# Kernel tuning notes

Measured on AMD Instinct MI355X. Metric: run time of the kernel, lower is better.

The kernel has to match this reference:

```python
import jax, jax.numpy as jnp
import numpy as np

B, S, D, H, V = 4, 1024, 1024, 16, 1024
HD = D // H  # head_dim = 64
FF = 4 * D


def _layer_norm(x, g, b, eps=1e-5):
    mu = jnp.mean(x, axis=-1, keepdims=True)
    var = jnp.var(x, axis=-1, keepdims=True)
    return (x - mu) * jax.lax.rsqrt(var + eps) * g + b


def _pos_encoding(seq_len, d_model):
    # sinusoidal PE, matching PositionalEncoding buffer construction
    pos = jnp.arange(seq_len, dtype=jnp.float32)[:, None]
    div = jnp.exp(jnp.arange(0, d_model, 2, dtype=jnp.float32) * (-np.log(10000.0) / d_model))
    pe = jnp.zeros((seq_len, d_model), dtype=jnp.float32)
    pe = pe.at[:, 0::2].set(jnp.sin(pos * div))
    pe = pe.at[:, 1::2].set(jnp.cos(pos * div))
    return pe


def setup_inputs() -> dict:
    key = jax.random.key(0)
    ks = jax.random.split(key, 12)
    sc = 0.02
    return {
        "inputs": jax.random.randint(ks[0], (B, S), 0, V, dtype=jnp.int32),
        "targets": jax.random.randint(ks[1], (B, S), 0, V, dtype=jnp.int32),
        "wte": jax.random.normal(ks[2], (V, D), jnp.float32) * sc,
        "wq": jax.random.normal(ks[3], (D, D), jnp.float32) * sc,
        "bq": jnp.zeros((D,), jnp.float32),
        "wk": jax.random.normal(ks[4], (D, D), jnp.float32) * sc,
        "bk": jnp.zeros((D,), jnp.float32),
        "wv": jax.random.normal(ks[5], (D, D), jnp.float32) * sc,
        "bv": jnp.zeros((D,), jnp.float32),
        "wo": jax.random.normal(ks[6], (D, D), jnp.float32) * sc,
        "bo": jnp.zeros((D,), jnp.float32),
        "w1": jax.random.normal(ks[7], (D, FF), jnp.float32) * sc,
        "b1": jnp.zeros((FF,), jnp.float32),
        "w2": jax.random.normal(ks[8], (FF, D), jnp.float32) * sc,
        "b2": jnp.zeros((D,), jnp.float32),
        "ln1_g": jnp.ones((D,), jnp.float32),
        "ln1_b": jnp.zeros((D,), jnp.float32),
        "ln2_g": jnp.ones((D,), jnp.float32),
        "ln2_b": jnp.zeros((D,), jnp.float32),
    }


def reference(inputs, targets, wte, wq, bq, wk, bk, wv, bv, wo, bo,
              w1, b1, w2, b2, ln1_g, ln1_b, ln2_g, ln2_b):
    # embedding + positional encoding
    x = wte[inputs] + _pos_encoding(S, D)  # [B,S,D]

    # naive causal multi-head attention (dropout = identity in eval)
    q = (x @ wq + bq).reshape(B, S, H, HD)
    k = (x @ wk + bk).reshape(B, S, H, HD)
    v = (x @ wv + bv).reshape(B, S, H, HD)
    scores = jnp.einsum('bqhd,bkhd->bhqk', q, k) / np.sqrt(HD)  # [B,H,S,S]
    causal = jnp.tril(jnp.ones((S, S), dtype=bool))
    scores = jnp.where(causal, scores, -jnp.inf)
    attn = jax.nn.softmax(scores, axis=-1)
    ctx = jnp.einsum('bhqk,bkhd->bqhd', attn, v).reshape(B, S, D)
    att_out = ctx @ wo + bo

    # residual + LN1, FFN + GELU, residual + LN2
    adn = _layer_norm(x + att_out, ln1_g, ln1_b)
    h = jax.nn.gelu(adn @ w1 + b1, approximate=False) @ w2 + b2
    logits = _layer_norm(h + adn, ln2_g, ln2_b)

    # cross-entropy over d_model(=vocab) classes
    logits_flat = logits.reshape(B * S, D)
    tgt = targets.reshape(B * S)
    logp = jax.nn.log_softmax(logits_flat, axis=-1)
    loss = -jnp.mean(jnp.take_along_axis(logp, tgt[:, None], axis=-1))
    return logits_flat, loss
```

## Files before the change

kernel.cpp:

```cpp
#include <hip/hip_runtime.h>
#include <math.h>

#define BB 4
#define SS 1024
#define DD 1024
#define HH 16
#define HDIM 64
#define FF 4096
#define MM 4096

typedef short bf16x8 __attribute__((ext_vector_type(8)));
typedef short bf16x4 __attribute__((ext_vector_type(4)));
typedef float f32x4  __attribute__((ext_vector_type(4)));

static __device__ __forceinline__ short f2bf(float f){
  unsigned u = __float_as_uint(f);
  u += 0x7FFFu + ((u >> 16) & 1u);
  return (short)(u >> 16);
}
static __device__ __forceinline__ float b2f(short s){
  return __uint_as_float(((unsigned)(unsigned short)s) << 16);
}

static __device__ __forceinline__ float erf_fast(float x){
  float ax = fabsf(x);
  float t  = __builtin_amdgcn_rcpf(1.0f + 0.3275911f * ax);
  float p  = t * (0.254829592f + t * (-0.284496736f + t * (1.421413741f +
             t * (-1.453152027f + t * 1.061405429f))));
  float e  = 1.0f - p * __expf(-ax * ax);
  return copysignf(e, x);
}

static __device__ __forceinline__ void gl_lds16(const short* g, short* l){
  __builtin_amdgcn_global_load_lds((const __attribute__((address_space(1))) unsigned int*)g,
                                   (__attribute__((address_space(3))) unsigned int*)l,
                                   16, 0, 0);
}

__global__ __launch_bounds__(256) void trans_all_kernel(
    const float* __restrict__ wq, const float* __restrict__ wk,
    const float* __restrict__ wv, const float* __restrict__ wo,
    const float* __restrict__ w1, const float* __restrict__ w2,
    short* __restrict__ wqkvt, short* __restrict__ wot,
    short* __restrict__ w1t,   short* __restrict__ w2t){
  __shared__ float t[32][33];
  int idx = blockIdx.x;
  const float* src; short* dst; int R, C, cx, ry;
  if (idx < 4096){
    int wsel = idx >> 10, tt = idx & 1023;
    cx = tt & 31; ry = tt >> 5; R = 1024; C = 1024;
    src = (wsel == 0) ? wq : (wsel == 1) ? wk : (wsel == 2) ? wv : wo;
    dst = (wsel == 3) ? wot : wqkvt + (size_t)wsel * 1024 * 1024;
  } else if (idx < 8192){
    int tt = idx - 4096; cx = tt & 127; ry = tt >> 7; R = 1024; C = 4096;
    src = w1; dst = w1t;
  } else {
    int tt = idx - 8192; cx = tt & 31; ry = tt >> 5; R = 4096; C = 1024;
    src = w2; dst = w2t;
  }
  int c0 = cx * 32, r0 = ry * 32;
  int tx = threadIdx.x, ty = threadIdx.y;
#pragma unroll
  for (int i = 0; i < 32; i += 8)
    t[ty + i][tx] = src[(size_t)(r0 + ty + i) * C + (c0 + tx)];
  __syncthreads();
#pragma unroll
  for (int i = 0; i < 32; i += 8)
    dst[(size_t)(c0 + ty + i) * R + (r0 + tx)] = f2bf(t[tx][ty + i]);
}

__global__ __launch_bounds__(256) void concat_bias_kernel(const float* __restrict__ a,
                                                          const float* __restrict__ b,
                                                          const float* __restrict__ c,
                                                          float* __restrict__ dst){
  int t = blockIdx.x * 256 + threadIdx.x;
  float v = (t < 1024) ? a[t] : (t < 2048 ? b[t - 1024] : c[t - 2048]);
  dst[t] = v;
}

__global__ __launch_bounds__(256) void embed_kernel(const int* __restrict__ inputs,
                                                    const float* __restrict__ wte,
                                                    short* __restrict__ xb){
  int idx4 = blockIdx.x * 256 + threadIdx.x;
  int row = idx4 >> 8;
  int d   = (idx4 & 255) * 4;
  int s   = row & (SS - 1);
  int tok = inputs[row];
  float4 w = *(const float4*)&wte[(size_t)tok * DD + d];
  const float cdiv = -9.210340371976184f / 512.0f;
  int i0 = d >> 1;
  float ang0 = (float)s * expf((float)i0 * cdiv);
  float ang1 = (float)s * expf((float)(i0 + 1) * cdiv);
  float x0 = w.x + sinf(ang0);
  float x1 = w.y + cosf(ang0);
  float x2 = w.z + sinf(ang1);
  float x3 = w.w + cosf(ang1);
  bf16x4 sb; sb[0]=f2bf(x0); sb[1]=f2bf(x1); sb[2]=f2bf(x2); sb[3]=f2bf(x3);
  *(bf16x4*)&xb[(size_t)row * DD + d] = sb;
}

template<int MODE, bool GELU, bool ADDBIAS>
__global__ __launch_bounds__(512) void gemm256_kernel(const short* __restrict__ A,
    const short* __restrict__ Bt, const float* __restrict__ bias,
    short* __restrict__ o0, short* __restrict__ o1,
    short* __restrict__ o2, short* __restrict__ o3,
    short* __restrict__ qo, short* __restrict__ ko, short* __restrict__ vto,
    int M, int N, int K, int Kc){
  __shared__ __align__(16) short lds[4][2][8192];
  int tid = threadIdx.x;
  int lid = blockIdx.y * gridDim.x + blockIdx.x;
  int cpx = (gridDim.x * gridDim.y) >> 3;
  int swz = (lid & 7) * cpx + (lid >> 3);
  int n0 = (swz % gridDim.x) * 256;
  int m0 = (swz / gridDim.x) * 256;
  int bz = blockIdx.z;
  int kbeg = bz * Kc;
  int w = tid >> 6, lane = tid & 63, lr = lane & 15, lg = lane >> 4;
  int wm = w >> 2, wn = w & 3;
  f32x4 acc[8][4] = {};

  int srow = w * 16 + (lane >> 2);
  int scol = (((lane & 3) ^ ((lane >> 3) & 3)) * 8);
  const short* Arow = A  + (size_t)(m0 + srow) * K + kbeg + scol;
  const short* Brow = Bt + (size_t)(n0 + srow) * K + kbeg + scol;

  auto STAGE = [&](int buf, int kt){
    int k0 = kt * 32;
#pragma unroll
    for (int j = 0; j < 2; j++){
      gl_lds16(Arow + (size_t)(j * 128) * K + k0, &lds[buf][0][j * 4096 + w * 512]);
      gl_lds16(Brow + (size_t)(j * 128) * K + k0, &lds[buf][1][j * 4096 + w * 512]);
    }
  };

  int nst = Kc >> 5;
  STAGE(0, 0);
  if (nst > 1) STAGE(1, 1);
  if (nst > 2) STAGE(2, 2);

  int axor = ((lr >> 1) & 3) << 4;

  for (int it = 0; it < nst; it++){
    if (it + 3 < nst) STAGE((it + 3) & 3, it + 3);
    if (it + 3 < nst)      asm volatile("s_waitcnt vmcnt(12)" ::: "memory");
    else if (it + 2 < nst) asm volatile("s_waitcnt vmcnt(8)"  ::: "memory");
    else if (it + 1 < nst) asm volatile("s_waitcnt vmcnt(4)"  ::: "memory");
    else                   asm volatile("s_waitcnt vmcnt(0)"  ::: "memory");
    __builtin_amdgcn_s_barrier();

    const short* la = &lds[it & 3][0][0];
    const short* lb = &lds[it & 3][1][0];
    bf16x8 bfrag[4], afrag[8];
#pragma unroll
    for (int ni = 0; ni < 4; ni++){
      int off = ((((wn * 64 + ni * 16 + lr) * 64) + lg * 16) ^ axor) >> 1;
      bfrag[ni] = *(const bf16x8*)&lb[off];
    }
#pragma unroll
    for (int mi = 0; mi < 8; mi++){
      int off = ((((wm * 128 + mi * 16 + lr) * 64) + lg * 16) ^ axor) >> 1;
      afrag[mi] = *(const bf16x8*)&la[off];
    }
    __builtin_amdgcn_s_setprio(1);
#pragma unroll
    for (int mi = 0; mi < 8; mi++)
#pragma unroll
      for (int ni = 0; ni < 4; ni++)
        acc[mi][ni] = __builtin_amdgcn_mfma_f32_16x16x32_bf16(afrag[mi], bfrag[ni], acc[mi][ni], 0, 0, 0);
    __builtin_amdgcn_s_setprio(0);
    asm volatile("" ::: "memory");
    __builtin_amdgcn_s_barrier();
  }

  short* slab = (MODE == 1) ? ((bz == 0) ? o0 : (bz == 1) ? o1 : (bz == 2) ? o2 : o3) : o0;
  bool addb = ADDBIAS && (MODE != 1 || bz == 0);
#pragma unroll
  for (int mi = 0; mi < 8; mi++){
#pragma unroll
    for (int ni = 0; ni < 4; ni++){
      int ng = n0 + wn * 64 + ni * 16 + lr;
      float bv = addb ? bias[ng] : 0.0f;
      int mg0 = m0 + wm * 128 + mi * 16 + 4 * lg;
      if (MODE == 2){
        int sel = n0 >> 10;
        if (sel == 2){
          int d = ng & 1023; int hh = d >> 6, nn = d & 63;
          int bI = mg0 >> 10, sI = mg0 & 1023;
          bf16x4 pk;
#pragma unroll
          for (int r = 0; r < 4; r++) pk[r] = f2bf(acc[mi][ni][r] + bv);
          *(bf16x4*)&vto[(((size_t)(bI * HH + hh)) * HDIM + nn) * SS + sI] = pk;
        } else {
          short* dst = (sel == 0) ? qo : ko;
#pragma unroll
          for (int r = 0; r < 4; r++)
            dst[(size_t)(mg0 + r) * DD + (ng & 1023)] = f2bf(acc[mi][ni][r] + bv);
        }
      } else {
#pragma unroll
        for (int r = 0; r < 4; r++){
          float v = acc[mi][ni][r] + bv;
          if (GELU) v = 0.5f * v * (1.0f + erf_fast(v * 0.70710678118654752f));
          slab[(size_t)(mg0 + r) * N + ng] = f2bf(v);
        }
      }
    }
  }
}

__global__ __launch_bounds__(256) void attn_kernel(const short* __restrict__ qb,
                                                   const short* __restrict__ kb,
                                                   const short* __restrict__ vtb,
                                                   short* __restrict__ ctxb){
  __shared__ __align__(16) short k_lds[2][64 * 64];
  __shared__ __align__(16) short v_lds[2][64 * 64];
  __shared__ __align__(16) short p_lds[4][2][16 * 72];
  int qp = blockIdx.x, h = blockIdx.y, b = blockIdx.z;
  int Tlo = qp, Thi = 15 - qp;
  int tid = threadIdx.x, w = tid >> 6, lane = tid & 63, lr = lane & 15, lg = lane >> 4;

  const short* kp0 = kb  + (size_t)b * SS * DD + h * HDIM;
  const short* vt0 = vtb + (size_t)(b * HH + h) * HDIM * SS;

  bf16x8 qf0[2], qf1[2];
#pragma unroll
  for (int ti = 0; ti < 2; ti++){
    int T = ti ? Thi : Tlo;
    const short* qp_ = qb + ((size_t)(b * SS + T * 64 + w * 16 + lr) * DD + h * HDIM);
    qf0[ti] = *(const bf16x8*)&qp_[lg * 8];
    qf1[ti] = *(const bf16x8*)&qp_[32 + lg * 8];
  }

  float m[2][4], l[2][4];
  f32x4 acc[2][4] = {};
#pragma unroll
  for (int ti = 0; ti < 2; ti++)
#pragma unroll
    for (int r = 0; r < 4; r++){ m[ti][r] = -1e30f; l[ti][r] = 0.0f; }

  int srow8 = lane >> 3;
  int sjs   = (lane & 7) ^ srow8;
  auto STAGE = [&](int buf, int kt){
#pragma unroll
    for (int i = 0; i < 2; i++){
      int rb  = (w + 4 * i) * 8;
      int row = rb + srow8;
      gl_lds16(kp0 + (size_t)(kt * 64 + row) * DD + sjs * 8, &k_lds[buf][rb * 64]);
      gl_lds16(vt0 + (size_t)row * SS + kt * 64 + sjs * 8,   &v_lds[buf][rb * 64]);
    }
  };

  int cur = 0;
  STAGE(0, 0);
  asm volatile("s_waitcnt vmcnt(0)" ::: "memory");
  __syncthreads();

  bf16x8 pf0[2], pf1[2];
  for (int kt = 0; kt <= Thi; kt++){
    if (kt < Thi) STAGE(cur ^ 1, kt + 1);

    bf16x8 kf0[4], kf1[4];
#pragma unroll
    for (int sub = 0; sub < 4; sub++){
      int r = sub * 16 + lr;
      kf0[sub] = *(const bf16x8*)&k_lds[cur][r * 64 + ((lg     ^ (r & 7)) * 8)];
      kf1[sub] = *(const bf16x8*)&k_lds[cur][r * 64 + (((lg+4) ^ (r & 7)) * 8)];
    }

#pragma unroll
    for (int ti = 0; ti < 2; ti++){
      int T = ti ? Thi : Tlo;
      if (kt > T) continue;
      f32x4 sc4[4];
#pragma unroll
      for (int sub = 0; sub < 4; sub++){
        f32x4 t = {};
        t = __builtin_amdgcn_mfma_f32_16x16x32_bf16(qf0[ti], kf0[sub], t, 0, 0, 0);
        t = __builtin_amdgcn_mfma_f32_16x16x32_bf16(qf1[ti], kf1[sub], t, 0, 0, 0);
#pragma unroll
        for (int r = 0; r < 4; r++) t[r] *= 0.125f;
        sc4[sub] = t;
      }
      if (kt == T){
#pragma unroll
        for (int sub = 0; sub < 4; sub++)
#pragma unroll
          for (int r = 0; r < 4; r++)
            if (16 * sub + lr > 16 * w + 4 * lg + r) sc4[sub][r] = -1e30f;
      }

      float pm[4];
#pragma unroll
      for (int r = 0; r < 4; r++)
        pm[r] = fmaxf(fmaxf(sc4[0][r], sc4[1][r]), fmaxf(sc4[2][r], sc4[3][r]));
#pragma unroll
      for (int off = 1; off < 16; off <<= 1)
#pragma unroll
        for (int r = 0; r < 4; r++) pm[r] = fmaxf(pm[r], __shfl_xor(pm[r], off));

      float scl[4], rs[4];
#pragma unroll
      for (int r = 0; r < 4; r++){
        float mn = fmaxf(m[ti][r], pm[r]);
        scl[r] = __expf(m[ti][r] - mn);
        m[ti][r] = mn;
        rs[r] = 0.0f;
      }
#pragma unroll
      for (int sub = 0; sub < 4; sub++)
#pragma unroll
        for (int r = 0; r < 4; r++){
          float p = __expf(sc4[sub][r] - m[ti][r]);
          sc4[sub][r] = p;
          rs[r] += p;
        }
#pragma unroll
      for (int off = 1; off < 16; off <<= 1)
#pragma unroll
        for (int r = 0; r < 4; r++) rs[r] += __shfl_xor(rs[r], off);
#pragma unroll
      for (int r = 0; r < 4; r++) l[ti][r] = l[ti][r] * scl[r] + rs[r];
#pragma unroll
      for (int nb = 0; nb < 4; nb++)
#pragma unroll
        for (int r = 0; r < 4; r++) acc[ti][nb][r] *= scl[r];

      short* pw = &p_lds[w][ti][0];
#pragma unroll
      for (int sub = 0; sub < 4; sub++)
#pragma unroll
        for (int r = 0; r < 4; r++)
          pw[(4 * lg + r) * 72 + sub * 16 + lr] = f2bf(sc4[sub][r]);
      pf0[ti] = *(const bf16x8*)&pw[lr * 72 + lg * 8];
      pf1[ti] = *(const bf16x8*)&pw[lr * 72 + 32 + lg * 8];
    }

    bf16x8 vf0[4], vf1[4];
#pragma unroll
    for (int nb = 0; nb < 4; nb++){
      int r = nb * 16 + lr;
      vf0[nb] = *(const bf16x8*)&v_lds[cur][r * 64 + ((lg     ^ (r & 7)) * 8)];
      vf1[nb] = *(const bf16x8*)&v_lds[cur][r * 64 + (((lg+4) ^ (r & 7)) * 8)];
    }

#pragma unroll
    for (int ti = 0; ti < 2; ti++){
      int T = ti ? Thi : Tlo;
      if (kt > T) continue;
#pragma unroll
      for (int nb = 0; nb < 4; nb++){
        acc[ti][nb] = __builtin_amdgcn_mfma_f32_16x16x32_bf16(pf0[ti], vf0[nb], acc[ti][nb], 0, 0, 0);
        acc[ti][nb] = __builtin_amdgcn_mfma_f32_16x16x32_bf16(pf1[ti], vf1[nb], acc[ti][nb], 0, 0, 0);
      }
    }

    asm volatile("s_waitcnt vmcnt(0)" ::: "memory");
    __syncthreads();
    cur ^= 1;
  }

#pragma unroll
  for (int ti = 0; ti < 2; ti++){
    int T = ti ? Thi : Tlo;
#pragma unroll
    for (int r = 0; r < 4; r++){
      float inv = 1.0f / l[ti][r];
      int row = T * 64 + w * 16 + 4 * lg + r;
#pragma unroll
      for (int nb = 0; nb < 4; nb++)
        ctxb[(size_t)(b * SS + row) * DD + h * HDIM + nb * 16 + lr] = f2bf(acc[ti][nb][r] * inv);
    }
  }
}

template<int NPART, bool WF32, bool LOSS>
__global__ __launch_bounds__(256) void ln_kernel(const short* __restrict__ p0,
                                                 const short* __restrict__ p1,
                                                 const short* __restrict__ p2,
                                                 const short* __restrict__ p3,
                                                 const short* __restrict__ resb,
                                                 const float* __restrict__ g,
                                                 const float* __restrict__ be,
                                                 float* __restrict__ of,
                                                 short* __restrict__ ob,
                                                 const int* __restrict__ tgt,
                                                 float* __restrict__ lrow){
  int row = blockIdx.x, tid = threadIdx.x;
  size_t base = (size_t)row * DD + tid * 4;
  bf16x4 rv = *(const bf16x4*)&resb[base];
  float x0 = b2f(rv[0]), x1 = b2f(rv[1]), x2 = b2f(rv[2]), x3 = b2f(rv[3]);
  const short* ps[4] = {p0, p1, p2, p3};
#pragma unroll
  for (int p = 0; p < NPART; p++){
    bf16x4 pv = *(const bf16x4*)&ps[p][base];
    x0 += b2f(pv[0]); x1 += b2f(pv[1]); x2 += b2f(pv[2]); x3 += b2f(pv[3]);
  }
  float s = x0 + x1 + x2 + x3;
  float q = x0 * x0 + x1 * x1 + x2 * x2 + x3 * x3;
#pragma unroll
  for (int off = 32; off; off >>= 1){ s += __shfl_xor(s, off); q += __shfl_xor(q, off); }
  __shared__ float red[9];
  if ((tid & 63) == 0){ red[tid >> 6] = s; red[4 + (tid >> 6)] = q; }
  __syncthreads();
  s = red[0] + red[1] + red[2] + red[3];
  q = red[4] + red[5] + red[6] + red[7];
  float mean = s * (1.0f / DD);
  float var  = q * (1.0f / DD) - mean * mean;
  float rstd = rsqrtf(var + 1e-5f);
  float4 gv  = *(const float4*)&g[tid * 4];
  float4 bev = *(const float4*)&be[tid * 4];
  float y0 = (x0 - mean) * rstd * gv.x + bev.x;
  float y1 = (x1 - mean) * rstd * gv.y + bev.y;
  float y2 = (x2 - mean) * rstd * gv.z + bev.z;
  float y3 = (x3 - mean) * rstd * gv.w + bev.w;
  if (WF32){
    *(float4*)&of[base] = make_float4(y0, y1, y2, y3);
  } else {
    bf16x4 sb; sb[0]=f2bf(y0); sb[1]=f2bf(y1); sb[2]=f2bf(y2); sb[3]=f2bf(y3);
    *(bf16x4*)&ob[base] = sb;
  }
  if (LOSS){
    __syncthreads();
    float mx = fmaxf(fmaxf(y0, y1), fmaxf(y2, y3));
#pragma unroll
    for (int off = 32; off; off >>= 1) mx = fmaxf(mx, __shfl_xor(mx, off));
    if ((tid & 63) == 0) red[tid >> 6] = mx;
    int t = tgt[row];
    if (tid == (t >> 2))
      red[8] = ((t & 3) == 0) ? y0 : ((t & 3) == 1) ? y1 : ((t & 3) == 2) ? y2 : y3;
    __syncthreads();
    mx = fmaxf(fmaxf(red[0], red[1]), fmaxf(red[2], red[3]));
    float se = __expf(y0 - mx) + __expf(y1 - mx) + __expf(y2 - mx) + __expf(y3 - mx);
#pragma unroll
    for (int off = 32; off; off >>= 1) se += __shfl_xor(se, off);
    if ((tid & 63) == 0) red[4 + (tid >> 6)] = se;
    __syncthreads();
    if (tid == 0){
      float tot = red[4] + red[5] + red[6] + red[7];
      lrow[row] = mx + logf(tot) - red[8];
    }
  }
}

__global__ __launch_bounds__(256) void loss_reduce_kernel(const float* __restrict__ pr,
                                                          float* __restrict__ outp){
  int tid = threadIdx.x;
  float s = 0.0f;
  for (int i = tid; i < MM; i += 256) s += pr[i];
#pragma unroll
  for (int off = 32; off; off >>= 1) s += __shfl_xor(s, off);
  __shared__ float red[4];
  if ((tid & 63) == 0) red[tid >> 6] = s;
  __syncthreads();
  if (tid == 0) outp[0] = (red[0] + red[1] + red[2] + red[3]) * (1.0f / MM);
}

extern "C" void kernel_launch(void* const* d_in, const int* in_sizes, int n_in,
                              void* d_out, int out_size, void* d_ws, size_t ws_size,
                              hipStream_t stream){
  const int*   inputs  = (const int*)  d_in[0];
  const int*   targets = (const int*)  d_in[1];
  const float* wte     = (const float*)d_in[2];
  const float* wq      = (const float*)d_in[3];
  const float* bq      = (const float*)d_in[4];
  const float* wk      = (const float*)d_in[5];
  const float* bk      = (const float*)d_in[6];
  const float* wv      = (const float*)d_in[7];
  const float* bvv     = (const float*)d_in[8];
  const float* wo      = (const float*)d_in[9];
  const float* bo      = (const float*)d_in[10];
  const float* w1      = (const float*)d_in[11];
  const float* b1      = (const float*)d_in[12];
  const float* w2      = (const float*)d_in[13];
  const float* b2      = (const float*)d_in[14];
  const float* ln1g    = (const float*)d_in[15];
  const float* ln1b    = (const float*)d_in[16];
  const float* ln2g    = (const float*)d_in[17];
  const float* ln2b    = (const float*)d_in[18];
  float* out = (float*)d_out;

  char* ws = (char*)d_ws;
  const size_t MB = 1024 * 1024;
  short* wqkvt = (short*)(ws + 0 * MB);
  short* wot   = (short*)(ws + 6 * MB);
  short* w1t   = (short*)(ws + 8 * MB);
  short* w2t   = (short*)(ws + 16 * MB);
  short* xb    = (short*)(ws + 24 * MB);
  short* qbuf  = (short*)(ws + 32 * MB);
  short* kbuf  = (short*)(ws + 40 * MB);
  short* vtb   = (short*)(ws + 48 * MB);
  short* ctxb  = (short*)(ws + 56 * MB);
  short* pr0   = (short*)(ws + 64 * MB);
  short* pr1   = (short*)(ws + 72 * MB);
  short* pr2   = (short*)(ws + 80 * MB);
  short* pr3   = (short*)(ws + 88 * MB);
  short* adnb  = (short*)(ws + 96 * MB);
  short* h1b   = (short*)(ws + 32 * MB);
  short* hs0   = (short*)(ws + 64 * MB);
  short* hs1   = (short*)(ws + 72 * MB);
  short* hs2   = (short*)(ws + 80 * MB);
  short* hs3   = (short*)(ws + 88 * MB);
  float* lrow  = (float*)(ws + 104 * MB);
  float* bqkv  = (float*)(ws + 105 * MB);

  trans_all_kernel<<<12288, dim3(32, 8), 0, stream>>>(
      wq, wk, wv, wo, w1, w2, wqkvt, wot, w1t, w2t);
  concat_bias_kernel<<<12, 256, 0, stream>>>(bq, bk, bvv, bqkv);

  embed_kernel<<<4096, 256, 0, stream>>>(inputs, wte, xb);

  gemm256_kernel<2, false, true><<<dim3(12, 16), 512, 0, stream>>>(
      xb, wqkvt, bqkv, nullptr, nullptr, nullptr, nullptr,
      qbuf, kbuf, vtb, MM, 3 * DD, DD, DD);

  attn_kernel<<<dim3(8, 16, 4), 256, 0, stream>>>(qbuf, kbuf, vtb, ctxb);

  gemm256_kernel<1, false, true><<<dim3(4, 16, 4), 512, 0, stream>>>(
      ctxb, wot, bo, pr0, pr1, pr2, pr3,
      nullptr, nullptr, nullptr, MM, DD, DD, 256);

  ln_kernel<4, false, false><<<4096, 256, 0, stream>>>(
      pr0, pr1, pr2, pr3, xb, ln1g, ln1b, nullptr, adnb, nullptr, nullptr);

  gemm256_kernel<0, true, true><<<dim3(16, 16), 512, 0, stream>>>(
      adnb, w1t, b1, h1b, nullptr, nullptr, nullptr,
      nullptr, nullptr, nullptr, MM, FF, DD, DD);

  gemm256_kernel<1, false, true><<<dim3(4, 16, 4), 512, 0, stream>>>(
      h1b, w2t, b2, hs0, hs1, hs2, hs3,
      nullptr, nullptr, nullptr, MM, DD, FF, 1024);

  ln_kernel<4, true, true><<<4096, 256, 0, stream>>>(
      hs0, hs1, hs2, hs3, adnb, ln2g, ln2b, out, nullptr, targets, lrow);

  loss_reduce_kernel<<<1, 256, 0, stream>>>(lrow, out + (size_t)MM * DD);
}
```

Before: 237.1 us.

## Double-buffer GEMM fragments in registers and use one barrier per k-step

The GEMM main loop now loads the next k-step's A/B fragments from LDS into a second register set while the MFMAs for the current step run. Each iteration now has one barrier instead of two, and the LDS fragment offsets are computed once before the loop. The launch bounds also ask for two blocks per CU, which caps registers per thread. That cap could force spills, since the accumulators and two fragment sets are held at once, and 128 KB of LDS per block may prevent two blocks from fitting on a CU anyway. The loop also assumes at least three k-stages and an even stage count.

After: 229.4 us. 3.3% less time.

```diff
diff --git a/kernel.cpp b/kernel.cpp
--- a/kernel.cpp
+++ b/kernel.cpp
@@ -100,7 +100,7 @@
 }
 
 template<int MODE, bool GELU, bool ADDBIAS>
-__global__ __launch_bounds__(512) void gemm256_kernel(const short* __restrict__ A,
+__global__ __launch_bounds__(512, 2) void gemm256_kernel(const short* __restrict__ A,
     const short* __restrict__ Bt, const float* __restrict__ bias,
     short* __restrict__ o0, short* __restrict__ o1,
     short* __restrict__ o2, short* __restrict__ o3,
@@ -135,42 +135,55 @@
 
   int nst = Kc >> 5;
   STAGE(0, 0);
-  if (nst > 1) STAGE(1, 1);
-  if (nst > 2) STAGE(2, 2);
+  STAGE(1, 1);
+  STAGE(2, 2);
 
   int axor = ((lr >> 1) & 3) << 4;
-
-  for (int it = 0; it < nst; it++){
-    if (it + 3 < nst) STAGE((it + 3) & 3, it + 3);
-    if (it + 3 < nst)      asm volatile("s_waitcnt vmcnt(12)" ::: "memory");
-    else if (it + 2 < nst) asm volatile("s_waitcnt vmcnt(8)"  ::: "memory");
-    else if (it + 1 < nst) asm volatile("s_waitcnt vmcnt(4)"  ::: "memory");
-    else                   asm volatile("s_waitcnt vmcnt(0)"  ::: "memory");
-    __builtin_amdgcn_s_barrier();
-
-    const short* la = &lds[it & 3][0][0];
-    const short* lb = &lds[it & 3][1][0];
-    bf16x8 bfrag[4], afrag[8];
-#pragma unroll
-    for (int ni = 0; ni < 4; ni++){
-      int off = ((((wn * 64 + ni * 16 + lr) * 64) + lg * 16) ^ axor) >> 1;
-      bfrag[ni] = *(const bf16x8*)&lb[off];
-    }
-#pragma unroll
-    for (int mi = 0; mi < 8; mi++){
-      int off = ((((wm * 128 + mi * 16 + lr) * 64) + lg * 16) ^ axor) >> 1;
-      afrag[mi] = *(const bf16x8*)&la[off];
-    }
-    __builtin_amdgcn_s_setprio(1);
-#pragma unroll
-    for (int mi = 0; mi < 8; mi++)
-#pragma unroll
-      for (int ni = 0; ni < 4; ni++)
-        acc[mi][ni] = __builtin_amdgcn_mfma_f32_16x16x32_bf16(afrag[mi], bfrag[ni], acc[mi][ni], 0, 0, 0);
-    __builtin_amdgcn_s_setprio(0);
-    asm volatile("" ::: "memory");
-    __builtin_amdgcn_s_barrier();
-  }
+  int boff[4], aoff[8];
+#pragma unroll
+  for (int ni = 0; ni < 4; ni++)
+    boff[ni] = ((((wn * 64 + ni * 16 + lr) * 64) + lg * 16) ^ axor) >> 1;
+#pragma unroll
+  for (int mi = 0; mi < 8; mi++)
+    aoff[mi] = ((((wm * 128 + mi * 16 + lr) * 64) + lg * 16) ^ axor) >> 1;
+
+#define FRAGS_READ(BUF, AF, BF)                                           \
+  { const short* la_ = &lds[BUF][0][0];                                   \
+    const short* lb_ = &lds[BUF][1][0];                                   \
+    _Pragma("unroll")                                                     \
+    for (int ni_ = 0; ni_ < 4; ni_++) BF[ni_] = *(const bf16x8*)&lb_[boff[ni_]]; \
+    _Pragma("unroll")                                                     \
+    for (int mi_ = 0; mi_ < 8; mi_++) AF[mi_] = *(const bf16x8*)&la_[aoff[mi_]]; }
+
+#define GITER(IT, AC, BC, AN, BN)                                         \
+  { int it_ = (IT);                                                       \
+    if (it_ + 3 < nst) STAGE((it_ + 3) & 3, it_ + 3);                     \
+    if (it_ + 1 < nst) FRAGS_READ((it_ + 1) & 3, AN, BN);                 \
+    __builtin_amdgcn_s_setprio(1);                                        \
+    _Pragma("unroll")                                                     \
+    for (int mi_ = 0; mi_ < 8; mi_++)                                     \
+      _Pragma("unroll")                                                   \
+      for (int ni_ = 0; ni_ < 4; ni_++)                                   \
+        acc[mi_][ni_] = __builtin_amdgcn_mfma_f32_16x16x32_bf16(AC[mi_], BC[ni_], acc[mi_][ni_], 0, 0, 0); \
+    __builtin_amdgcn_s_setprio(0);                                        \
+    if (it_ + 3 < nst) asm volatile("s_waitcnt vmcnt(4)" ::: "memory");   \
+    else               asm volatile("s_waitcnt vmcnt(0)" ::: "memory");   \
+    asm volatile("s_waitcnt lgkmcnt(0)" ::: "memory");                    \
+    __builtin_amdgcn_s_barrier();                                         \
+    asm volatile("" ::: "memory"); }
+
+  asm volatile("s_waitcnt vmcnt(4)" ::: "memory");
+  __builtin_amdgcn_s_barrier();
+  asm volatile("" ::: "memory");
+
+  bf16x8 aA[8], bA[4], aB[8], bB[4];
+  FRAGS_READ(0, aA, bA);
+  for (int it = 0; it < nst; it += 2){
+    GITER(it,     aA, bA, aB, bB);
+    GITER(it + 1, aB, bB, aA, bA);
+  }
+#undef GITER
+#undef FRAGS_READ
 
   short* slab = (MODE == 1) ? ((bz == 0) ? o0 : (bz == 1) ? o1 : (bz == 2) ? o2 : o3) : o0;
   bool addb = ADDBIAS && (MODE != 1 || bz == 0);
```

## Restructure 256x256 GEMM main loop into quadrant-staged double-buffered K=64 pipeline

Applied to the files above, without the earlier changes.

Rewrites the GEMM main loop to use K-tiles of 64 with two LDS buffers, each split into A/B half-tiles. Each iteration runs four MFMA quadrant phases, and the prefetch for tile t+2 is interleaved between phases so global-to-LDS loads overlap compute. The LDS swizzle and fragment layout change to an XOR pattern over 8-element chunks. Launch bounds now request two blocks per CU. This adds many more barriers per iteration and risks register pressure or spills under the occupancy hint, and the buffer-reuse timing needs care to avoid read/write races.

Measured after the change: 233.5 us. Within noise of the previous version (-1.5%).

```diff
diff --git a/kernel.cpp b/kernel.cpp
--- a/kernel.cpp
+++ b/kernel.cpp
@@ -36,6 +36,8 @@
                                    (__attribute__((address_space(3))) unsigned int*)l,
                                    16, 0, 0);
 }
+
+#define MFMA_BF16 __builtin_amdgcn_mfma_f32_16x16x32_bf16
 
 __global__ __launch_bounds__(256) void trans_all_kernel(
     const float* __restrict__ wq, const float* __restrict__ wk,
@@ -100,13 +102,13 @@
 }
 
 template<int MODE, bool GELU, bool ADDBIAS>
-__global__ __launch_bounds__(512) void gemm256_kernel(const short* __restrict__ A,
+__global__ __launch_bounds__(512, 2) void gemm256_kernel(const short* __restrict__ A,
     const short* __restrict__ Bt, const float* __restrict__ bias,
     short* __restrict__ o0, short* __restrict__ o1,
     short* __restrict__ o2, short* __restrict__ o3,
     short* __restrict__ qo, short* __restrict__ ko, short* __restrict__ vto,
     int M, int N, int K, int Kc){
-  __shared__ __align__(16) short lds[4][2][8192];
+  __shared__ __align__(16) short lds[8 * 8192];
   int tid = threadIdx.x;
   int lid = blockIdx.y * gridDim.x + blockIdx.x;
   int cpx = (gridDim.x * gridDim.y) >> 3;
@@ -119,56 +121,114 @@
   int wm = w >> 2, wn = w & 3;
   f32x4 acc[8][4] = {};
 
-  int srow = w * 16 + (lane >> 2);
-  int scol = (((lane & 3) ^ ((lane >> 3) & 3)) * 8);
-  const short* Arow = A  + (size_t)(m0 + srow) * K + kbeg + scol;
-  const short* Brow = Bt + (size_t)(n0 + srow) * K + kbeg + scol;
-
-  auto STAGE = [&](int buf, int kt){
-    int k0 = kt * 32;
-#pragma unroll
-    for (int j = 0; j < 2; j++){
-      gl_lds16(Arow + (size_t)(j * 128) * K + k0, &lds[buf][0][j * 4096 + w * 512]);
-      gl_lds16(Brow + (size_t)(j * 128) * K + k0, &lds[buf][1][j * 4096 + w * 512]);
-    }
+  int sr = lane >> 3;
+  int sg = (lane & 7) ^ sr;
+  auto STAGE_HALF = [&](int buf, int typ, int half, int kt){
+    const short* s0 = (typ ? Bt : A) + (size_t)kbeg + sg * 8;
+    int rb = (typ ? n0 : m0) + half * 128 + w * 8 + sr;
+#pragma unroll
+    for (int j = 0; j < 2; j++)
+      gl_lds16(s0 + (size_t)(rb + j * 64) * K + kt * 64,
+               &lds[(((buf << 2) | (typ << 1) | half) << 13) + (j << 12) + (w << 9)]);
   };
 
-  int nst = Kc >> 5;
-  STAGE(0, 0);
-  if (nst > 1) STAGE(1, 1);
-  if (nst > 2) STAGE(2, 2);
-
-  int axor = ((lr >> 1) & 3) << 4;
-
-  for (int it = 0; it < nst; it++){
-    if (it + 3 < nst) STAGE((it + 3) & 3, it + 3);
-    if (it + 3 < nst)      asm volatile("s_waitcnt vmcnt(12)" ::: "memory");
-    else if (it + 2 < nst) asm volatile("s_waitcnt vmcnt(8)"  ::: "memory");
-    else if (it + 1 < nst) asm volatile("s_waitcnt vmcnt(4)"  ::: "memory");
-    else                   asm volatile("s_waitcnt vmcnt(0)"  ::: "memory");
-    __builtin_amdgcn_s_barrier();
-
-    const short* la = &lds[it & 3][0][0];
-    const short* lb = &lds[it & 3][1][0];
-    bf16x8 bfrag[4], afrag[8];
-#pragma unroll
-    for (int ni = 0; ni < 4; ni++){
-      int off = ((((wn * 64 + ni * 16 + lr) * 64) + lg * 16) ^ axor) >> 1;
-      bfrag[ni] = *(const bf16x8*)&lb[off];
-    }
-#pragma unroll
-    for (int mi = 0; mi < 8; mi++){
-      int off = ((((wm * 128 + mi * 16 + lr) * 64) + lg * 16) ^ axor) >> 1;
-      afrag[mi] = *(const bf16x8*)&la[off];
-    }
+  int nt = Kc >> 6;
+  STAGE_HALF(0, 0, 0, 0); STAGE_HALF(0, 0, 1, 0);
+  STAGE_HALF(0, 1, 0, 0); STAGE_HALF(0, 1, 1, 0);
+  STAGE_HALF(1, 0, 0, 1); STAGE_HALF(1, 0, 1, 1);
+  STAGE_HALF(1, 1, 0, 1); STAGE_HALF(1, 1, 1, 1);
+  asm volatile("s_waitcnt vmcnt(8)" ::: "memory");
+  __builtin_amdgcn_s_barrier();
+
+  int lr64 = lr * 64;
+  int ck0 = ((lg     ) ^ (lr & 7)) * 8;
+  int ck1 = ((lg + 4 ) ^ (lr & 7)) * 8;
+  int brow = (wn & 1) << 12;
+
+  bf16x8 Alo[4][2], Ahi[4][2], Blo[2][2], Bhi[2][2];
+
+  for (int t = 0; t < nt; t++){
+    int b = t & 1;
+    int abase = (((b << 2) | wm) << 13) + lr64;
+    int bbase = (((b << 2) | 2 | (wn >> 1)) << 13) + brow + lr64;
+
+#pragma unroll
+    for (int fi = 0; fi < 4; fi++){
+      Alo[fi][0] = *(const bf16x8*)&lds[abase + fi * 1024 + ck0];
+      Alo[fi][1] = *(const bf16x8*)&lds[abase + fi * 1024 + ck1];
+    }
+#pragma unroll
+    for (int ni = 0; ni < 2; ni++){
+      Blo[ni][0] = *(const bf16x8*)&lds[bbase + ni * 1024 + ck0];
+      Blo[ni][1] = *(const bf16x8*)&lds[bbase + ni * 1024 + ck1];
+    }
+    __builtin_amdgcn_s_barrier();
+    asm volatile("s_waitcnt lgkmcnt(0)" ::: "memory");
+    __builtin_amdgcn_sched_barrier(0);
     __builtin_amdgcn_s_setprio(1);
 #pragma unroll
-    for (int mi = 0; mi < 8; mi++)
-#pragma unroll
-      for (int ni = 0; ni < 4; ni++)
-        acc[mi][ni] = __builtin_amdgcn_mfma_f32_16x16x32_bf16(afrag[mi], bfrag[ni], acc[mi][ni], 0, 0, 0);
+    for (int mi = 0; mi < 4; mi++)
+#pragma unroll
+      for (int ni = 0; ni < 2; ni++){
+        acc[mi][ni] = MFMA_BF16(Alo[mi][0], Blo[ni][0], acc[mi][ni], 0, 0, 0);
+        acc[mi][ni] = MFMA_BF16(Alo[mi][1], Blo[ni][1], acc[mi][ni], 0, 0, 0);
+      }
     __builtin_amdgcn_s_setprio(0);
-    asm volatile("" ::: "memory");
+    __builtin_amdgcn_s_barrier();
+
+#pragma unroll
+    for (int fi = 0; fi < 4; fi++){
+      Ahi[fi][0] = *(const bf16x8*)&lds[abase + (fi + 4) * 1024 + ck0];
+      Ahi[fi][1] = *(const bf16x8*)&lds[abase + (fi + 4) * 1024 + ck1];
+    }
+    __builtin_amdgcn_s_barrier();
+    asm volatile("s_waitcnt lgkmcnt(0)" ::: "memory");
+    __builtin_amdgcn_sched_barrier(0);
+    __builtin_amdgcn_s_setprio(1);
+#pragma unroll
+    for (int mi = 0; mi < 4; mi++)
+#pragma unroll
+      for (int ni = 0; ni < 2; ni++){
+        acc[mi + 4][ni] = MFMA_BF16(Ahi[mi][0], Blo[ni][0], acc[mi + 4][ni], 0, 0, 0);
+        acc[mi + 4][ni] = MFMA_BF16(Ahi[mi][1], Blo[ni][1], acc[mi + 4][ni], 0, 0, 0);
+      }
+    __builtin_amdgcn_s_setprio(0);
+    __builtin_amdgcn_s_barrier();
+
+#pragma unroll
+    for (int ni = 0; ni < 2; ni++){
+      Bhi[ni][0] = *(const bf16x8*)&lds[bbase + (ni + 2) * 1024 + ck0];
+      Bhi[ni][1] = *(const bf16x8*)&lds[bbase + (ni + 2) * 1024 + ck1];
+    }
+    if (t + 2 < nt){ STAGE_HALF(b, 0, 0, t + 2); STAGE_HALF(b, 0, 1, t + 2); }
+    __builtin_amdgcn_s_barrier();
+    asm volatile("s_waitcnt lgkmcnt(0)" ::: "memory");
+    __builtin_amdgcn_sched_barrier(0);
+    __builtin_amdgcn_s_setprio(1);
+#pragma unroll
+    for (int mi = 0; mi < 4; mi++)
+#pragma unroll
+      for (int ni = 0; ni < 2; ni++){
+        acc[mi + 4][ni + 2] = MFMA_BF16(Ahi[mi][0], Bhi[ni][0], acc[mi + 4][ni + 2], 0, 0, 0);
+        acc[mi + 4][ni + 2] = MFMA_BF16(Ahi[mi][1], Bhi[ni][1], acc[mi + 4][ni + 2], 0, 0, 0);
+      }
+    __builtin_amdgcn_s_setprio(0);
+    __builtin_amdgcn_s_barrier();
+
+    if (t + 2 < nt){ STAGE_HALF(b, 1, 0, t + 2); STAGE_HALF(b, 1, 1, t + 2); }
+    __builtin_amdgcn_s_barrier();
+    __builtin_amdgcn_sched_barrier(0);
+    __builtin_amdgcn_s_setprio(1);
+#pragma unroll
+    for (int mi = 0; mi < 4; mi++)
+#pragma unroll
+      for (int ni = 0; ni < 2; ni++){
+        acc[mi][ni + 2] = MFMA_BF16(Alo[mi][0], Bhi[ni][0], acc[mi][ni + 2], 0, 0, 0);
+        acc[mi][ni + 2] = MFMA_BF16(Alo[mi][1], Bhi[ni][1], acc[mi][ni + 2], 0, 0, 0);
+      }
+    __builtin_amdgcn_s_setprio(0);
+    if (t == nt - 2) asm volatile("s_waitcnt vmcnt(0)" ::: "memory");
+    else             asm volatile("s_waitcnt vmcnt(8)" ::: "memory");
     __builtin_amdgcn_s_barrier();
   }
 
@@ -275,8 +335,8 @@
 #pragma unroll
       for (int sub = 0; sub < 4; sub++){
         f32x4 t = {};
-        t = __builtin_amdgcn_mfma_f32_16x16x32_bf16(qf0[ti], kf0[sub], t, 0, 0, 0);
-        t = __builtin_amdgcn_mfma_f32_16x16x32_bf16(qf1[ti], kf1[sub], t, 0, 0, 0);
+        t = MFMA_BF16(qf0[ti], kf0[sub], t, 0, 0, 0);
+        t = MFMA_BF16(qf1[ti], kf1[sub], t, 0, 0, 0);
 #pragma unroll
         for (int r = 0; r < 4; r++) t[r] *= 0.125f;
         sc4[sub] = t;
@@ -349,8 +409,8 @@
       if (kt > T) continue;
 #pragma unroll
       for (int nb = 0; nb < 4; nb++){
-        acc[ti][nb] = __builtin_amdgcn_mfma_f32_16x16x32_bf16(pf0[ti], vf0[nb], acc[ti][nb], 0, 0, 0);
-        acc[ti][nb] = __builtin_amdgcn_mfma_f32_16x16x32_bf16(pf1[ti], vf1[nb], acc[ti][nb], 0, 0, 0);
+        acc[ti][nb] = MFMA_BF16(pf0[ti], vf0[nb], acc[ti][nb], 0, 0, 0);
+        acc[ti][nb] = MFMA_BF16(pf1[ti], vf1[nb], acc[ti][nb], 0, 0, 0);
       }
     }
 
```
